# Optimization experiments

Measured on AMD Instinct MI355X. Metric: run time of the kernel, lower is better.

Reference implementation:

```python
import jax, jax.numpy as jnp
import numpy as np

D_MODEL = 1024
NUM_HEADS = 16
HEAD_DIM = D_MODEL // NUM_HEADS


def setup_inputs() -> dict:
    key = jax.random.key(0)
    ks = jax.random.split(key, 5)
    s = 1.0 / np.sqrt(D_MODEL)
    return {
        "x": jax.random.normal(ks[0], (2, 2048, D_MODEL), dtype=jnp.float32),
        "Wqkv": jax.random.normal(ks[1], (3 * D_MODEL, D_MODEL), dtype=jnp.float32) * s,
        "bqkv": jax.random.normal(ks[2], (3 * D_MODEL,), dtype=jnp.float32) * s,
        "Wo": jax.random.normal(ks[3], (D_MODEL, D_MODEL), dtype=jnp.float32) * s,
        "bo": jax.random.normal(ks[4], (D_MODEL,), dtype=jnp.float32) * s,
    }


def reference(x, Wqkv, bqkv, Wo, bo):
    B, S, D = x.shape
    H, hd = NUM_HEADS, HEAD_DIM
    # fused QKV projection (torch Linear: x @ W.T + b)
    qkv = x @ Wqkv.T + bqkv                      # [B, S, 3D]
    qkv = qkv.reshape(B, S, H, 3 * hd).transpose(0, 2, 1, 3)  # [B, H, S, 3hd]
    q, k, v = jnp.split(qkv, 3, axis=-1)         # each [B, H, S, hd]
    scaled = jnp.einsum("bhqd,bhkd->bhqk", q, k) / jnp.sqrt(jnp.float32(hd))
    # module applies causal mask when its `mask` flag is False (the default)
    causal = jnp.tril(jnp.ones((S, S), dtype=bool))
    scaled = jnp.where(causal, scaled, -jnp.inf)
    attn = jax.nn.softmax(scaled, axis=-1)       # [B, H, S, S]
    values = jnp.einsum("bhqk,bhkd->bhqd", attn, v)  # [B, H, S, hd]
    # NOTE: original uses .reshape (not transpose-then-reshape) on the
    # [B, H, S, hd] tensor directly — reproduce that exact layout.
    values = values.reshape(B, S, H * hd)
    out = values @ Wo.T + bo                     # [B, S, D]
    return out
```

## Files before the change

kernel.cpp:

```cpp
#include <hip/hip_runtime.h>

typedef __attribute__((ext_vector_type(8))) short bf16x8;
typedef __attribute__((ext_vector_type(4))) float f32x4;

#define D_MODEL 1024
#define NHEADS 16
#define HDIM 64
#define SEQ 2048
#define BATCH 2
#define MROWS (BATCH*SEQ)
#define NQKV (3*D_MODEL)
#define QSCALE 0.1803368801111204f
#define CSTR 144

__device__ __forceinline__ unsigned short f2bf(float f) {
  unsigned int u = __float_as_uint(f);
  u += 0x7FFF + ((u >> 16) & 1);
  return (unsigned short)(u >> 16);
}
__device__ __forceinline__ unsigned int pack2bf(float a, float b) {
#if __has_builtin(__builtin_amdgcn_cvt_pk_bf16_f32)
  auto r = __builtin_amdgcn_cvt_pk_bf16_f32(a, b);
  unsigned int u; __builtin_memcpy(&u, &r, 4);
  return u;
#else
  return ((unsigned int)f2bf(b) << 16) | (unsigned int)f2bf(a);
#endif
}

__device__ __forceinline__ void gload16(const void* g, void* l) {
  __builtin_amdgcn_global_load_lds((const __attribute__((address_space(1))) void*)g,
                                   (__attribute__((address_space(3))) void*)l, 16, 0, 0);
}

#define N4_X     1048576
#define N4_WQKV   786432
#define N4_WO     262144
__global__ void cvt_all_kernel(const float4* __restrict__ x,
                               const float4* __restrict__ wqkv,
                               const float4* __restrict__ wo,
                               ushort4* __restrict__ xb,
                               ushort4* __restrict__ wqkvb,
                               ushort4* __restrict__ wob) {
  int i = blockIdx.x * blockDim.x + threadIdx.x;
  const float4* s; ushort4* d; int j;
  if (i < N4_X)                { s = x;    d = xb;    j = i; }
  else if (i < N4_X + N4_WQKV) { s = wqkv; d = wqkvb; j = i - N4_X; }
  else                         { s = wo;   d = wob;   j = i - (N4_X + N4_WQKV); }
  float4 v = s[j];
  ushort4 o;
  o.x = f2bf(v.x); o.y = f2bf(v.y); o.z = f2bf(v.z); o.w = f2bf(v.w);
  d[j] = o;
}

template<int MODE, int BM>
__global__ __launch_bounds__(256) void gemm_bt_kernel(
    const unsigned short* __restrict__ A,
    const unsigned short* __restrict__ Bm,
    const float* __restrict__ bias,
    float* __restrict__ outF,
    unsigned short* __restrict__ Qb,
    unsigned short* __restrict__ Kb,
    unsigned short* __restrict__ VTb,
    int M, int N, int K)
{
  constexpr int MI = BM / 32;
  constexpr int STG = BM*32 + 128*32;
  constexpr int SHSZ = (MODE == 0 && 128*CSTR > 2*STG) ? 128*CSTR : 2*STG;
  __shared__ __align__(16) unsigned short Sh[SHSZ];
  const int tid = threadIdx.x;
  const int wave = tid >> 6, lane = tid & 63;
  const int lm = lane & 15, quad = lane >> 4;
  const int wm = (wave >> 1) * (BM/2), wn = (wave & 1) * 64;
  const int m0 = blockIdx.y * BM, n0 = blockIdx.x * 128;

  f32x4 acc[MI][4] = {};

  auto stage_in = [&](int k0, int sb) {
    unsigned short* As = Sh + sb*STG;
    unsigned short* Bs = As + BM*32;
#pragma unroll
    for (int i = 0; i < BM/64; i++) {
      int ch = i*256 + tid;
      int r = ch >> 2, cg = (ch & 3) ^ ((r >> 1) & 3);
      gload16(&A[(size_t)(m0 + r) * K + k0 + cg*8], &As[ch*8]);
    }
#pragma unroll
    for (int i = 0; i < 2; i++) {
      int ch = i*256 + tid;
      int r = ch >> 2, cg = (ch & 3) ^ ((r >> 1) & 3);
      gload16(&Bm[(size_t)(n0 + r) * K + k0 + cg*8], &Bs[ch*8]);
    }
  };

  stage_in(0, 0);
  for (int k0 = 0; k0 < K; k0 += 32) {
    const int cur = (k0 >> 5) & 1;
    __syncthreads();
    if (k0 + 32 < K) stage_in(k0 + 32, cur ^ 1);
    const unsigned short* As = Sh + cur*STG;
    const unsigned short* Bs = As + BM*32;
    bf16x8 af[MI], bfr[4];
#pragma unroll
    for (int mi = 0; mi < MI; mi++) {
      int r = wm + mi*16 + lm;
      af[mi] = *(const bf16x8*)&As[(r*4 + (quad ^ ((r >> 1) & 3))) * 8];
    }
#pragma unroll
    for (int ni = 0; ni < 4; ni++) {
      int r = wn + ni*16 + lm;
      bfr[ni] = *(const bf16x8*)&Bs[(r*4 + (quad ^ ((r >> 1) & 3))) * 8];
    }
#pragma unroll
    for (int mi = 0; mi < MI; mi++)
#pragma unroll
      for (int ni = 0; ni < 4; ni++)
        acc[mi][ni] = __builtin_amdgcn_mfma_f32_16x16x32_bf16(af[mi], bfr[ni], acc[mi][ni], 0, 0, 0);
  }

  if (MODE == 1) {
#pragma unroll
    for (int mi = 0; mi < MI; mi++)
#pragma unroll
      for (int ni = 0; ni < 4; ni++)
#pragma unroll
        for (int r = 0; r < 4; r++) {
          int row = m0 + wm + mi*16 + quad*4 + r;
          int col = n0 + wn + ni*16 + lm;
          outF[(size_t)row * N + col] = acc[mi][ni][r] + bias[col];
        }
  } else {
    __syncthreads();
#pragma unroll
    for (int mi = 0; mi < MI; mi++)
#pragma unroll
      for (int ni = 0; ni < 4; ni++)
#pragma unroll
        for (int r = 0; r < 4; r++) {
          int row_l = wm + mi*16 + quad*4 + r;
          int col_l = wn + ni*16 + lm;
          int col = n0 + col_l;
          float v = acc[mi][ni][r] + bias[col];
          if (((col % 192) >> 6) == 0) v *= QSCALE;
          Sh[row_l*CSTR + col_l] = f2bf(v);
        }
    __syncthreads();
#pragma unroll
    for (int i = 0; i < 8; i++) {
      int lin = i*256 + tid;
      int row_l = lin >> 4, cc = (lin & 15) * 8;
      int col = n0 + cc;
      int h = col / 192, rr = col - h*192;
      int ty = rr >> 6, e = rr & 63;
      if (ty < 2) {
        uint4 d = *(const uint4*)&Sh[row_l*CSTR + cc];
        int row = m0 + row_l;
        int b = row >> 11, s = row & (SEQ - 1);
        unsigned short* dst = ty ? Kb : Qb;
        *(uint4*)&dst[((size_t)(b*NHEADS + h)*SEQ + s)*HDIM + e] = d;
      }
    }
#pragma unroll
    for (int i = 0; i < 8; i++) {
      int lin = i*256 + tid;
      int col_l = lin & 127, s8 = (lin >> 7) * 8;
      int col = n0 + col_l;
      int h = col / 192, rr = col - h*192;
      if ((rr >> 6) == 2) {
        int e = rr & 63;
        unsigned short tmp[8];
#pragma unroll
        for (int j = 0; j < 8; j++) tmp[j] = Sh[(s8 + j)*CSTR + col_l];
        int row = m0 + s8;
        int b = row >> 11, s = row & (SEQ - 1);
        size_t vb = ((size_t)(b*NHEADS + h)*HDIM + e)*SEQ;
        int pos = (s & ~31) | (((s >> 2) & 3) << 3) | (((s >> 4) & 1) << 2);
        *(uint2*)&VTb[vb + pos]     = *(const uint2*)&tmp[0];
        *(uint2*)&VTb[vb + pos + 8] = *(const uint2*)&tmp[4];
      }
    }
  }
}

__global__ __launch_bounds__(256, 2) void flash_attn_kernel(
    const unsigned short* __restrict__ Qb,
    const unsigned short* __restrict__ Kb,
    const unsigned short* __restrict__ VTb,
    unsigned short* __restrict__ Ob)
{
  const int tid = threadIdx.x;
  const int wave = tid >> 6, lane = tid & 63;
  const int lm = lane & 15, quad = lane >> 4;
  const int bx = blockIdx.x;
  const int bh = (bx & 7) * 4 + (bx >> 3);
  const int pr = blockIdx.y;
  const int t0 = 15 - pr, t1 = pr;
  const int nk0 = t0 + 1;
  const int ntot = nk0 + t1 + 1;

  __shared__ __align__(16) unsigned short Ks[2][128*64];
  __shared__ __align__(16) unsigned short Vs[2][64*128];

  const unsigned short* Qbh  = Qb  + (size_t)bh*SEQ*HDIM;
  const unsigned short* Kbh  = Kb  + (size_t)bh*SEQ*HDIM;
  const unsigned short* VTbh = VTb + (size_t)bh*HDIM*SEQ;

  auto stage_in = [&](int k0, int sb) {
#pragma unroll
    for (int i = 0; i < 4; i++) {
      int ch = i*256 + tid;
      int r = ch >> 3, cg = (ch & 7) ^ (r & 7);
      gload16(&Kbh[(size_t)(k0 + r)*HDIM + cg*8], &Ks[sb][ch*8]);
    }
#pragma unroll
    for (int i = 0; i < 4; i++) {
      int ch = i*256 + tid;
      int e = ch >> 4, cg = (ch & 15) ^ (e & 7);
      gload16(&VTbh[(size_t)e*SEQ + k0 + cg*8], &Vs[sb][ch*8]);
    }
  };

  int rowq = t0*128 + wave*32;
  int query[2];
  bf16x8 qf[2][2];
#pragma unroll
  for (int g = 0; g < 2; g++) {
    query[g] = rowq + g*16 + lm;
#pragma unroll
    for (int kc = 0; kc < 2; kc++)
      qf[g][kc] = *(const bf16x8*)&Qbh[(size_t)query[g]*HDIM + kc*32 + quad*8];
  }

  f32x4 o[2][4] = {};
  float m_run[2] = {-1e30f, -1e30f}, l_run[2] = {0.f, 0.f};

  stage_in(0, 0);
  for (int s = 0; s < ntot; s++) {
    const int kt = (s < nk0) ? s : s - nk0;
    const int k0 = kt * 128;
    const int cur = s & 1;
    __syncthreads();
    if (s + 1 < ntot) {
      int sn = s + 1;
      int ktn = (sn < nk0) ? sn : sn - nk0;
      stage_in(ktn * 128, cur ^ 1);
    }

    f32x4 sc[2][8] = {};
    __builtin_amdgcn_s_setprio(1);
#pragma unroll
    for (int kc = 0; kc < 2; kc++)
#pragma unroll
      for (int mi = 0; mi < 8; mi++) {
        int r = mi*16 + lm, cc = kc*4 + quad;
        bf16x8 kf = *(const bf16x8*)&Ks[cur][(r*8 + (cc ^ (r & 7))) * 8];
        sc[0][mi] = __builtin_amdgcn_mfma_f32_16x16x32_bf16(kf, qf[0][kc], sc[0][mi], 0, 0, 0);
        sc[1][mi] = __builtin_amdgcn_mfma_f32_16x16x32_bf16(kf, qf[1][kc], sc[1][mi], 0, 0, 0);
      }
    __builtin_amdgcn_s_setprio(0);

    if (k0 + 127 > rowq) {
#pragma unroll
      for (int g = 0; g < 2; g++)
#pragma unroll
        for (int mi = 0; mi < 8; mi++)
#pragma unroll
          for (int r = 0; r < 4; r++) {
            int key = k0 + mi*16 + quad*4 + r;
            if (key > query[g]) sc[g][mi][r] = -1e30f;
          }
    }

    bf16x8 pf[2][4];
#pragma unroll
    for (int g = 0; g < 2; g++) {
      float tr8[8];
#pragma unroll
      for (int mi = 0; mi < 8; mi++)
        tr8[mi] = fmaxf(fmaxf(sc[g][mi][0], sc[g][mi][1]), fmaxf(sc[g][mi][2], sc[g][mi][3]));
#pragma unroll
      for (int st = 4; st > 0; st >>= 1)
#pragma unroll
        for (int j = 0; j < st; j++) tr8[j] = fmaxf(tr8[j], tr8[j + st]);
      float mx = tr8[0];
      mx = fmaxf(mx, __shfl_xor(mx, 16, 64));
      mx = fmaxf(mx, __shfl_xor(mx, 32, 64));
      float mnew = fmaxf(m_run[g], mx);
      float alpha = exp2f(m_run[g] - mnew);
      float p[8][4];
#pragma unroll
      for (int mi = 0; mi < 8; mi++)
#pragma unroll
        for (int r2 = 0; r2 < 4; r2++)
          p[mi][r2] = exp2f(sc[g][mi][r2] - mnew);
      float sr8[8];
#pragma unroll
      for (int mi = 0; mi < 8; mi++)
        sr8[mi] = (p[mi][0] + p[mi][1]) + (p[mi][2] + p[mi][3]);
#pragma unroll
      for (int st = 4; st > 0; st >>= 1)
#pragma unroll
        for (int j = 0; j < st; j++) sr8[j] += sr8[j + st];
      float rs = sr8[0];
      rs += __shfl_xor(rs, 16, 64);
      rs += __shfl_xor(rs, 32, 64);
      l_run[g] = l_run[g] * alpha + rs;
      if (__any(mnew != m_run[g])) {
#pragma unroll
        for (int ei = 0; ei < 4; ei++)
#pragma unroll
          for (int r2 = 0; r2 < 4; r2++) o[g][ei][r2] *= alpha;
      }
      m_run[g] = mnew;
#pragma unroll
      for (int kc = 0; kc < 4; kc++) {
        union { unsigned int w[4]; bf16x8 v; } pu;
        pu.w[0] = pack2bf(p[2*kc][0],   p[2*kc][1]);
        pu.w[1] = pack2bf(p[2*kc][2],   p[2*kc][3]);
        pu.w[2] = pack2bf(p[2*kc+1][0], p[2*kc+1][1]);
        pu.w[3] = pack2bf(p[2*kc+1][2], p[2*kc+1][3]);
        pf[g][kc] = pu.v;
      }
    }

    __builtin_amdgcn_s_setprio(1);
#pragma unroll
    for (int kc = 0; kc < 4; kc++)
#pragma unroll
      for (int ei = 0; ei < 4; ei++) {
        int e = ei*16 + lm, cc = kc*4 + quad;
        bf16x8 vf = *(const bf16x8*)&Vs[cur][(e*16 + (cc ^ (e & 7))) * 8];
        o[0][ei] = __builtin_amdgcn_mfma_f32_16x16x32_bf16(vf, pf[0][kc], o[0][ei], 0, 0, 0);
        o[1][ei] = __builtin_amdgcn_mfma_f32_16x16x32_bf16(vf, pf[1][kc], o[1][ei], 0, 0, 0);
      }
    __builtin_amdgcn_s_setprio(0);

    if (s == nk0 - 1 || s == ntot - 1) {
#pragma unroll
      for (int g = 0; g < 2; g++) {
        float inv = 1.0f / l_run[g];
        size_t obase = ((size_t)bh*SEQ + query[g]) * HDIM;
#pragma unroll
        for (int ei = 0; ei < 4; ei++) {
          uint2 u;
          u.x = pack2bf(o[g][ei][0]*inv, o[g][ei][1]*inv);
          u.y = pack2bf(o[g][ei][2]*inv, o[g][ei][3]*inv);
          *(uint2*)&Ob[obase + ei*16 + quad*4] = u;
        }
      }
      if (s == nk0 - 1) {
        rowq = t1*128 + wave*32;
#pragma unroll
        for (int g = 0; g < 2; g++) {
          query[g] = rowq + g*16 + lm;
#pragma unroll
          for (int kc = 0; kc < 2; kc++)
            qf[g][kc] = *(const bf16x8*)&Qbh[(size_t)query[g]*HDIM + kc*32 + quad*8];
#pragma unroll
          for (int ei = 0; ei < 4; ei++)
#pragma unroll
            for (int r2 = 0; r2 < 4; r2++) o[g][ei][r2] = 0.f;
          m_run[g] = -1e30f; l_run[g] = 0.f;
        }
      }
    }
  }
}

extern "C" void kernel_launch(void* const* d_in, const int* in_sizes, int n_in,
                              void* d_out, int out_size, void* d_ws, size_t ws_size,
                              hipStream_t stream) {
  const float* x    = (const float*)d_in[0];
  const float* Wqkv = (const float*)d_in[1];
  const float* bqkv = (const float*)d_in[2];
  const float* Wo   = (const float*)d_in[3];
  const float* bo   = (const float*)d_in[4];
  float* out = (float*)d_out;

  char* ws = (char*)d_ws;
  unsigned short* Xbf    = (unsigned short*)(ws);
  unsigned short* Wqkvbf = (unsigned short*)(ws + 8388608);
  unsigned short* Wobf   = (unsigned short*)(ws + 14680064);
  unsigned short* Qb     = (unsigned short*)(ws + 16777216);
  unsigned short* Kb     = (unsigned short*)(ws + 25165824);
  unsigned short* VTb    = (unsigned short*)(ws + 33554432);
  unsigned short* Ob     = (unsigned short*)(ws + 41943040);

  cvt_all_kernel<<<8192, 256, 0, stream>>>(
      (const float4*)x, (const float4*)Wqkv, (const float4*)Wo,
      (ushort4*)Xbf, (ushort4*)Wqkvbf, (ushort4*)Wobf);

  gemm_bt_kernel<0,128><<<dim3(24, 32), 256, 0, stream>>>(
      Xbf, Wqkvbf, bqkv, nullptr, Qb, Kb, VTb, MROWS, NQKV, D_MODEL);

  flash_attn_kernel<<<dim3(32, 8), 256, 0, stream>>>(Qb, Kb, VTb, Ob);

  gemm_bt_kernel<1,64><<<dim3(8, 64), 256, 0, stream>>>(
      Ob, Wobf, bo, out, nullptr, nullptr, nullptr, MROWS, D_MODEL, D_MODEL);
}
```

Measured before the change: 197.8 us.

## Split paired causal query tiles into separate blocks with one tile each

The attention kernel previously gave each block two query tiles (t and 15-t) so every block did the same amount of causal work. Now each block handles a single query tile, the grid doubles to 512 blocks, and the heavy tiles are ordered first (longest-first scheduling). This exposes more parallelism across the 256 CUs and removes the mid-loop Q reload and state reset, but block work becomes uneven and K/V tiles are staged more times in total.

```diff
diff --git a/kernel.cpp b/kernel.cpp
--- a/kernel.cpp
+++ b/kernel.cpp
@@ -193,10 +193,9 @@
   const int lm = lane & 15, quad = lane >> 4;
   const int bx = blockIdx.x;
   const int bh = (bx & 7) * 4 + (bx >> 3);
-  const int pr = blockIdx.y;
-  const int t0 = 15 - pr, t1 = pr;
-  const int nk0 = t0 + 1;
-  const int ntot = nk0 + t1 + 1;
+  const int by = blockIdx.y;
+  const int t  = (by < 8) ? (15 - by) : (by - 8);
+  const int nk = t + 1;
 
   __shared__ __align__(16) unsigned short Ks[2][128*64];
   __shared__ __align__(16) unsigned short Vs[2][64*128];
@@ -220,7 +219,7 @@
     }
   };
 
-  int rowq = t0*128 + wave*32;
+  const int rowq = t*128 + wave*32;
   int query[2];
   bf16x8 qf[2][2];
 #pragma unroll
@@ -235,16 +234,11 @@
   float m_run[2] = {-1e30f, -1e30f}, l_run[2] = {0.f, 0.f};
 
   stage_in(0, 0);
-  for (int s = 0; s < ntot; s++) {
-    const int kt = (s < nk0) ? s : s - nk0;
-    const int k0 = kt * 128;
+  for (int s = 0; s < nk; s++) {
+    const int k0 = s * 128;
     const int cur = s & 1;
     __syncthreads();
-    if (s + 1 < ntot) {
-      int sn = s + 1;
-      int ktn = (sn < nk0) ? sn : sn - nk0;
-      stage_in(ktn * 128, cur ^ 1);
-    }
+    if (s + 1 < nk) stage_in(k0 + 128, cur ^ 1);
 
     f32x4 sc[2][8] = {};
     __builtin_amdgcn_s_setprio(1);
@@ -334,35 +328,18 @@
         o[1][ei] = __builtin_amdgcn_mfma_f32_16x16x32_bf16(vf, pf[1][kc], o[1][ei], 0, 0, 0);
       }
     __builtin_amdgcn_s_setprio(0);
-
-    if (s == nk0 - 1 || s == ntot - 1) {
-#pragma unroll
-      for (int g = 0; g < 2; g++) {
-        float inv = 1.0f / l_run[g];
-        size_t obase = ((size_t)bh*SEQ + query[g]) * HDIM;
-#pragma unroll
-        for (int ei = 0; ei < 4; ei++) {
-          uint2 u;
-          u.x = pack2bf(o[g][ei][0]*inv, o[g][ei][1]*inv);
-          u.y = pack2bf(o[g][ei][2]*inv, o[g][ei][3]*inv);
-          *(uint2*)&Ob[obase + ei*16 + quad*4] = u;
-        }
-      }
-      if (s == nk0 - 1) {
-        rowq = t1*128 + wave*32;
-#pragma unroll
-        for (int g = 0; g < 2; g++) {
-          query[g] = rowq + g*16 + lm;
-#pragma unroll
-          for (int kc = 0; kc < 2; kc++)
-            qf[g][kc] = *(const bf16x8*)&Qbh[(size_t)query[g]*HDIM + kc*32 + quad*8];
-#pragma unroll
-          for (int ei = 0; ei < 4; ei++)
-#pragma unroll
-            for (int r2 = 0; r2 < 4; r2++) o[g][ei][r2] = 0.f;
-          m_run[g] = -1e30f; l_run[g] = 0.f;
-        }
-      }
+  }
+
+#pragma unroll
+  for (int g = 0; g < 2; g++) {
+    float inv = 1.0f / l_run[g];
+    size_t obase = ((size_t)bh*SEQ + query[g]) * HDIM;
+#pragma unroll
+    for (int ei = 0; ei < 4; ei++) {
+      uint2 u;
+      u.x = pack2bf(o[g][ei][0]*inv, o[g][ei][1]*inv);
+      u.y = pack2bf(o[g][ei][2]*inv, o[g][ei][3]*inv);
+      *(uint2*)&Ob[obase + ei*16 + quad*4] = u;
     }
   }
 }
@@ -393,7 +370,7 @@
   gemm_bt_kernel<0,128><<<dim3(24, 32), 256, 0, stream>>>(
       Xbf, Wqkvbf, bqkv, nullptr, Qb, Kb, VTb, MROWS, NQKV, D_MODEL);
 
-  flash_attn_kernel<<<dim3(32, 8), 256, 0, stream>>>(Qb, Kb, VTb, Ob);
+  flash_attn_kernel<<<dim3(32, 16), 256, 0, stream>>>(Qb, Kb, VTb, Ob);
 
   gemm_bt_kernel<1,64><<<dim3(8, 64), 256, 0, stream>>>(
       Ob, Wobf, bo, out, nullptr, nullptr, nullptr, MROWS, D_MODEL, D_MODEL);
```

After: 193.5 us. -2.2%, faster.
